# Performance work log

Measured on AMD Instinct MI355X. Metric: run time of the kernel, lower is better.

The kernel has to match this reference:

```python
import jax, jax.numpy as jnp
import numpy as np

M_TIME = 64      # signal model output length (time points)
N_DICT = 20000   # dictionary entries
B_VOX = 8192     # voxels / batch


def setup_inputs() -> dict:
    key = jax.random.key(0)
    k = jax.random.split(key, 6)
    input_real = jax.random.normal(k[0], (M_TIME, B_VOX), jnp.float32)
    input_imag = jax.random.normal(k[1], (M_TIME, B_VOX), jnp.float32)
    # raw dictionary signals, then normalize columns as append() does
    yr = jax.random.normal(k[2], (M_TIME, N_DICT), jnp.float32)
    yi = jax.random.normal(k[3], (M_TIME, N_DICT), jnp.float32)
    norm = jnp.sqrt(jnp.sum(yr * yr + yi * yi, axis=0))  # (N,)
    inverse_norm_y = 1.0 / norm
    y_real = yr * inverse_norm_y
    y_imag = yi * inverse_norm_y
    x_t1 = jax.random.uniform(k[4], (N_DICT,), jnp.float32, 0.1, 3.0)
    x_t2 = jax.random.uniform(k[5], (N_DICT,), jnp.float32, 0.01, 0.5)
    return {
        'input_real': input_real, 'input_imag': input_imag,
        'y_real': y_real, 'y_imag': y_imag,
        'inverse_norm_y': inverse_norm_y, 'x_t1': x_t1, 'x_t2': x_t2,
    }


def reference(input_real, input_imag, y_real, y_imag, inverse_norm_y, x_t1, x_t2):
    # |<y_n, s_b>|^2 for complex y and complex input, via 4 real GEMMs (as in the
    # original module): sim[n, b]
    sim = (jnp.einsum('mb,mn->nb', input_real, y_real) ** 2
           + jnp.einsum('mb,mn->nb', input_real, y_imag) ** 2
           + jnp.einsum('mb,mn->nb', input_imag, y_real) ** 2
           + jnp.einsum('mb,mn->nb', input_imag, y_imag) ** 2)
    idx = jnp.argmax(sim, axis=0)  # (B,)
    # scale = sum_m conj(y[:, idx]) * input * inverse_norm_y[idx]
    yr = y_real[:, idx]   # (M, B)
    yi = y_imag[:, idx]   # (M, B)
    inv = inverse_norm_y[idx]  # (B,)
    scale_r = jnp.sum(yr * input_real + yi * input_imag, axis=0) * inv
    scale_i = jnp.sum(yr * input_imag - yi * input_real, axis=0) * inv
    # returns (scale, t1, t2) with complex scale split into real/imag, stacked (4, B)
    return jnp.stack([scale_r, scale_i, x_t1[idx], x_t2[idx]])
```

## Files before the change

kernel.cpp:

```cpp
#include <hip/hip_runtime.h>
#include <hip/hip_bf16.h>
#include <stdint.h>

#define M_TIME 64
#define N_DICT 20000
#define B_VOX  8192

#define NTILES 313

typedef _Float16 v8h __attribute__((ext_vector_type(8)));
typedef float    v4f __attribute__((ext_vector_type(4)));
typedef float    v2f __attribute__((ext_vector_type(2)));

__device__ __forceinline__ unsigned long long u64max(unsigned long long a, unsigned long long b) { return a > b ? a : b; }
__device__ __forceinline__ unsigned umin32(unsigned a, unsigned b) { return a < b ? a : b; }
__device__ __forceinline__ unsigned umax32(unsigned a, unsigned b) { return a > b ? a : b; }
__device__ __forceinline__ unsigned umed3(unsigned a, unsigned b, unsigned c) {
    unsigned d;
    asm("v_med3_u32 %0, %1, %2, %3" : "=v"(d) : "v"(a), "v"(b), "v"(c));
    return d;
}

__global__ __launch_bounds__(256) void split_y(
    const float* __restrict__ yr, const float* __restrict__ yi,
    v8h* __restrict__ yp)
{
    const int u = blockIdx.x * 256 + threadIdx.x;
    const int n_l = u & 63;
    const int j   = (u >> 6) & 7;
    const int T   = (u >> 9) % NTILES;
    const int arr = u / (NTILES * 512);
    if (arr > 1) return;
    const float* P = arr ? yi : yr;
    const int n_g = T * 64 + n_l;
    v8h V;
#pragma unroll
    for (int c = 0; c < 8; ++c) {
        float v = 0.f;
        if (n_g < N_DICT) v = P[(j * 8 + c) * N_DICT + n_g];
        V[c] = (_Float16)v;
    }
    const int fr = (arr * 2 + (j >> 2)) * 4 + (j & 3);
    yp[((size_t)T * 16 + fr) * 64 + n_l] = V;
}

__global__ __launch_bounds__(256, 2) void gemm_pre(
    const float* __restrict__ ir, const float* __restrict__ ii,
    const v8h* __restrict__ yp,
    unsigned* __restrict__ cand, int tpc, int slots)
{
    __shared__ unsigned xm[4][4][16][2];

    const int tid  = threadIdx.x;
    const int wave = tid >> 6, lane = tid & 63;
    const int quad = lane >> 4, col = lane & 15;
    const int vox_w = blockIdx.x * 64;
    const int chunk = blockIdx.y;
    const int T0 = chunk * tpc;
    const int T1 = (T0 + tpc < NTILES) ? T0 + tpc : NTILES;

    v8h fh[2][4][2];
#pragma unroll
    for (int arr = 0; arr < 2; ++arr) {
        const float* P = arr ? ii : ir;
#pragma unroll
        for (int bt = 0; bt < 4; ++bt) {
            const int b = vox_w + bt * 16 + col;
#pragma unroll
            for (int h = 0; h < 2; ++h) {
                v8h H;
#pragma unroll
                for (int j = 0; j < 8; ++j) {
                    const int k = h * 32 + quad * 8 + j;
                    H[j] = (_Float16)P[k * B_VOX + b];
                }
                fh[arr][bt][h] = H;
            }
        }
    }

    v8h yf[2][2];
    auto loadf = [&](int T) {
        const v8h* yv = (const v8h*)((const char*)yp + (size_t)T * 16384);
        const int nrow = wave * 16 + col;
#pragma unroll
        for (int ri = 0; ri < 2; ++ri)
#pragma unroll
            for (int h = 0; h < 2; ++h)
                yf[ri][h] = yv[((ri * 2 + h) * 4 + quad) * 64 + nrow];
    };

    const v4f zc = {0.f, 0.f, 0.f, 0.f};
    unsigned t2a[4] = {0u, 0u, 0u, 0u}, t2b[4] = {0u, 0u, 0u, 0u};

    loadf(T0);
    for (int T = T0; T < T1; ++T) {
        const int tl = T - T0;
        v4f acc[4][4];
#define MF(A, B, C) __builtin_amdgcn_mfma_f32_16x16x32_f16(A, B, C, 0, 0, 0)
#pragma unroll
        for (int bt = 0; bt < 4; ++bt) {
            acc[bt][0] = MF(yf[0][0], fh[0][bt][0], zc);
            acc[bt][1] = MF(yf[1][0], fh[0][bt][0], zc);
            acc[bt][2] = MF(yf[0][0], fh[1][bt][0], zc);
            acc[bt][3] = MF(yf[1][0], fh[1][bt][0], zc);
        }
#pragma unroll
        for (int bt = 0; bt < 4; ++bt) {
            acc[bt][0] = MF(yf[0][1], fh[0][bt][1], acc[bt][0]);
            acc[bt][1] = MF(yf[1][1], fh[0][bt][1], acc[bt][1]);
            acc[bt][2] = MF(yf[0][1], fh[1][bt][1], acc[bt][2]);
            acc[bt][3] = MF(yf[1][1], fh[1][bt][1], acc[bt][3]);
        }
#undef MF
        if (T + 1 < T1) loadf(T + 1);

        const unsigned base = 0x1FFFu
            - (unsigned)(tl * 64 + wave * 16 + quad * 4);
#pragma unroll
        for (int bt = 0; bt < 4; ++bt) {
            v2f s01, s23;
            {
                const v2f p0 = __builtin_shufflevector(acc[bt][0], acc[bt][0], 0, 1);
                const v2f p1 = __builtin_shufflevector(acc[bt][1], acc[bt][1], 0, 1);
                const v2f p2 = __builtin_shufflevector(acc[bt][2], acc[bt][2], 0, 1);
                const v2f p3 = __builtin_shufflevector(acc[bt][3], acc[bt][3], 0, 1);
                v2f s = p0 * p0;
                s = __builtin_elementwise_fma(p1, p1, s);
                s = __builtin_elementwise_fma(p2, p2, s);
                s = __builtin_elementwise_fma(p3, p3, s);
                s01 = s;
            }
            {
                const v2f p0 = __builtin_shufflevector(acc[bt][0], acc[bt][0], 2, 3);
                const v2f p1 = __builtin_shufflevector(acc[bt][1], acc[bt][1], 2, 3);
                const v2f p2 = __builtin_shufflevector(acc[bt][2], acc[bt][2], 2, 3);
                const v2f p3 = __builtin_shufflevector(acc[bt][3], acc[bt][3], 2, 3);
                v2f s = p0 * p0;
                s = __builtin_elementwise_fma(p1, p1, s);
                s = __builtin_elementwise_fma(p2, p2, s);
                s = __builtin_elementwise_fma(p3, p3, s);
                s23 = s;
            }
#pragma unroll
            for (int r = 0; r < 4; ++r) {
                const float s = (r < 2) ? s01[r] : s23[r - 2];
                const unsigned pb = (__float_as_uint(s) & 0xFFFFE000u)
                                  | (base - (unsigned)r);
                const unsigned nb = umed3(pb, t2a[bt], t2b[bt]);
                t2a[bt] = umax32(pb, t2a[bt]);
                t2b[bt] = nb;
            }
        }
    }

    unsigned fa1[4], fa2[4];
#pragma unroll
    for (int bt = 0; bt < 4; ++bt) {
        unsigned a1 = t2a[bt], a2 = t2b[bt];
#pragma unroll
        for (int d = 16; d <= 32; d <<= 1) {
            unsigned b1 = (unsigned)__shfl_xor((int)a1, d, 64);
            unsigned b2 = (unsigned)__shfl_xor((int)a2, d, 64);
            unsigned mn = umin32(a1, b1);
            a1 = umax32(a1, b1);
            a2 = umax32(mn, umax32(a2, b2));
        }
        fa1[bt] = a1; fa2[bt] = a2;
    }
    if (lane < 16) {
#pragma unroll
        for (int bt = 0; bt < 4; ++bt) {
            xm[wave][bt][lane][0] = fa1[bt];
            xm[wave][bt][lane][1] = fa2[bt];
        }
    }
    __syncthreads();
    if (wave == 0 && lane < 16) {
#pragma unroll
        for (int bt = 0; bt < 4; ++bt) {
            unsigned m1 = 0u, m2 = 0u;
#pragma unroll
            for (int w = 0; w < 4; ++w) {
                const unsigned b1 = xm[w][bt][lane][0];
                const unsigned b2 = xm[w][bt][lane][1];
                m2 = umax32(m2, umax32(b2, umin32(m1, b1)));
                m1 = umax32(m1, b1);
            }
            const size_t vox = vox_w + bt * 16 + lane;
            cand[vox * slots + chunk * 2 + 0] = m1;
            cand[vox * slots + chunk * 2 + 1] = m2;
        }
    }
}

__global__ __launch_bounds__(256) void rescore_finish(
    const float* __restrict__ ir, const float* __restrict__ ii,
    const float* __restrict__ yr, const float* __restrict__ yi,
    const float* __restrict__ inv, const float* __restrict__ x1,
    const float* __restrict__ x2,
    const unsigned* __restrict__ cand, int slots, int tpc,
    float* __restrict__ out)
{
    const int tid  = threadIdx.x;
    const int vox  = blockIdx.x * 4 + (tid >> 6);
    const int slot = tid & 63;

    unsigned p = (slot < slots) ? cand[(size_t)vox * slots + slot] : 0u;
    float sa = __uint_as_float(p & 0xFFFFE000u);
    const int chunkc = slot >> 1;
    const int nn = chunkc * tpc * 64 + (0x1FFF - (int)(p & 0x1FFFu));

    float amax = sa;
#pragma unroll
    for (int d = 1; d <= 32; d <<= 1) amax = fmaxf(amax, __shfl_xor(amax, d, 64));

    unsigned long long q = 0ull;
    float rr = 0.f, ri = 0.f, s1 = 0.f, s2 = 0.f;
    const bool active = (slot < slots) && (nn >= 0) && (nn < N_DICT)
                     && (sa >= 0.97f * amax);
    if (active) {
        for (int m = 0; m < M_TIME; ++m) {
            float a  = yr[(size_t)m * N_DICT + nn];
            float c  = yi[(size_t)m * N_DICT + nn];
            float vr = ir[m * B_VOX + vox];
            float vi = ii[m * B_VOX + vox];
            rr = fmaf(vr, a, rr); ri = fmaf(vr, c, ri);
            s1 = fmaf(vi, a, s1); s2 = fmaf(vi, c, s2);
        }
        float s = fmaf(rr, rr, fmaf(ri, ri, fmaf(s1, s1, s2 * s2)));
        q = (((unsigned long long)__float_as_uint(s)) << 32)
          | (unsigned long long)(0xFFFFFFFFu - (unsigned)nn);
    }
    unsigned long long qm = q;
#pragma unroll
    for (int d = 1; d <= 32; d <<= 1) qm = u64max(qm, __shfl_xor(qm, d, 64));

    if (active && q == qm && qm != 0ull) {
        float ss = inv[nn];
        out[0 * B_VOX + vox] = (rr + s2) * ss;
        out[1 * B_VOX + vox] = (s1 - ri) * ss;
        out[2 * B_VOX + vox] = x1[nn];
        out[3 * B_VOX + vox] = x2[nn];
    }
}

__global__ __launch_bounds__(256, 3) void argmax_naive(
    const float* __restrict__ ir, const float* __restrict__ ii,
    const float* __restrict__ yr, const float* __restrict__ yi,
    int* __restrict__ idxout)
{
    int b = blockIdx.x * 256 + threadIdx.x;
    float bs = -1.0f; int bn = 0;
    for (int n = 0; n < N_DICT; ++n) {
        float a_rr = 0.f, a_ri = 0.f, a_s1 = 0.f, a_s2 = 0.f;
        for (int m = 0; m < M_TIME; ++m) {
            float a = yr[m * N_DICT + n], c = yi[m * N_DICT + n];
            float vr = ir[m * B_VOX + b], vi = ii[m * B_VOX + b];
            a_rr = fmaf(vr, a, a_rr); a_ri = fmaf(vr, c, a_ri);
            a_s1 = fmaf(vi, a, a_s1); a_s2 = fmaf(vi, c, a_s2);
        }
        float sim = fmaf(a_rr, a_rr, fmaf(a_ri, a_ri, fmaf(a_s1, a_s1, a_s2 * a_s2)));
        if (sim > bs) { bs = sim; bn = n; }
    }
    idxout[b] = bn;
}

__global__ void finish_k(const float* __restrict__ ir, const float* __restrict__ ii,
                         const float* __restrict__ yr, const float* __restrict__ yi,
                         const float* __restrict__ inv, const float* __restrict__ x1,
                         const float* __restrict__ x2,
                         const int* __restrict__ idxin, float* __restrict__ out)
{
    int b = blockIdx.x * blockDim.x + threadIdx.x;
    int idx = idxin[b];
    float ar = 0.f, ai = 0.f;
    for (int m = 0; m < M_TIME; ++m) {
        float a  = yr[(size_t)m * N_DICT + idx];
        float c  = yi[(size_t)m * N_DICT + idx];
        float vr = ir[m * B_VOX + b];
        float vi = ii[m * B_VOX + b];
        ar = fmaf(a, vr, ar); ar = fmaf(c, vi, ar);
        ai = fmaf(a, vi, ai); ai = fmaf(-c, vr, ai);
    }
    float s = inv[idx];
    out[0 * B_VOX + b] = ar * s;
    out[1 * B_VOX + b] = ai * s;
    out[2 * B_VOX + b] = x1[idx];
    out[3 * B_VOX + b] = x2[idx];
}

extern "C" void kernel_launch(void* const* d_in, const int* in_sizes, int n_in,
                              void* d_out, int out_size, void* d_ws, size_t ws_size,
                              hipStream_t stream) {
    const float* ir  = (const float*)d_in[0];
    const float* ii  = (const float*)d_in[1];
    const float* yr  = (const float*)d_in[2];
    const float* yi  = (const float*)d_in[3];
    const float* inv = (const float*)d_in[4];
    const float* x1  = (const float*)d_in[5];
    const float* x2  = (const float*)d_in[6];
    float* out = (float*)d_out;

    const size_t yp_bytes = (size_t)NTILES * 16384;

    int CH = 0;
    for (int c = 32; c >= 4; c >>= 1) {
        size_t cand_bytes = (size_t)B_VOX * (2 * c) * sizeof(unsigned);
        if (ws_size >= cand_bytes + yp_bytes) { CH = c; break; }
    }

    if (CH > 0) {
        const int slots = 2 * CH;
        const int tpc   = (NTILES + CH - 1) / CH;
        unsigned* cand = (unsigned*)d_ws;
        v8h* yp = (v8h*)((char*)d_ws + (size_t)B_VOX * slots * sizeof(unsigned));

        const int units = 2 * NTILES * 512;
        split_y<<<(units + 255) / 256, 256, 0, stream>>>(yr, yi, yp);
        gemm_pre<<<dim3(B_VOX / 64, CH), 256, 0, stream>>>(ir, ii, yp, cand, tpc, slots);
        rescore_finish<<<B_VOX / 4, 256, 0, stream>>>(ir, ii, yr, yi, inv, x1, x2,
                                                      cand, slots, tpc, out);
    } else {
        int* idxo = (int*)(out + 3 * B_VOX);
        argmax_naive<<<B_VOX / 256, 256, 0, stream>>>(ir, ii, yr, yi, idxo);
        finish_k<<<B_VOX / 256, 256, 0, stream>>>(ir, ii, yr, yi,
                                                  inv, x1, x2, idxo, out);
    }
}
```

Measured before the change: 186.2 us.

## Switch similarity GEMM to 32x32x16 MFMA with 2x2 wave tiling

```diff
diff --git a/kernel.cpp b/kernel.cpp
--- a/kernel.cpp
+++ b/kernel.cpp
@@ -11,6 +11,7 @@
 typedef _Float16 v8h __attribute__((ext_vector_type(8)));
 typedef float    v4f __attribute__((ext_vector_type(4)));
 typedef float    v2f __attribute__((ext_vector_type(2)));
+typedef float    v16f __attribute__((ext_vector_type(16)));
 
 __device__ __forceinline__ unsigned long long u64max(unsigned long long a, unsigned long long b) { return a > b ? a : b; }
 __device__ __forceinline__ unsigned umin32(unsigned a, unsigned b) { return a < b ? a : b; }
@@ -49,148 +50,126 @@
     const v8h* __restrict__ yp,
     unsigned* __restrict__ cand, int tpc, int slots)
 {
-    __shared__ unsigned xm[4][4][16][2];
+    __shared__ unsigned xm[2][32][2];
 
     const int tid  = threadIdx.x;
     const int wave = tid >> 6, lane = tid & 63;
-    const int quad = lane >> 4, col = lane & 15;
+    const int col  = lane & 31, hk = lane >> 5;
+    const int vh   = wave >> 1, nh = wave & 1;
     const int vox_w = blockIdx.x * 64;
     const int chunk = blockIdx.y;
     const int T0 = chunk * tpc;
     const int T1 = (T0 + tpc < NTILES) ? T0 + tpc : NTILES;
 
-    v8h fh[2][4][2];
+    v8h fh[2][4];
 #pragma unroll
     for (int arr = 0; arr < 2; ++arr) {
         const float* P = arr ? ii : ir;
-#pragma unroll
-        for (int bt = 0; bt < 4; ++bt) {
-            const int b = vox_w + bt * 16 + col;
-#pragma unroll
-            for (int h = 0; h < 2; ++h) {
-                v8h H;
-#pragma unroll
-                for (int j = 0; j < 8; ++j) {
-                    const int k = h * 32 + quad * 8 + j;
-                    H[j] = (_Float16)P[k * B_VOX + b];
-                }
-                fh[arr][bt][h] = H;
+        const int b = vox_w + vh * 32 + col;
+#pragma unroll
+        for (int ks = 0; ks < 4; ++ks) {
+            v8h H;
+#pragma unroll
+            for (int j = 0; j < 8; ++j) {
+                const int k = ks * 16 + hk * 8 + j;
+                H[j] = (_Float16)P[k * B_VOX + b];
             }
+            fh[arr][ks] = H;
         }
     }
 
-    v8h yf[2][2];
+    v8h yf[2][4];
     auto loadf = [&](int T) {
         const v8h* yv = (const v8h*)((const char*)yp + (size_t)T * 16384);
-        const int nrow = wave * 16 + col;
+        const int nr = nh * 32 + col;
 #pragma unroll
         for (int ri = 0; ri < 2; ++ri)
 #pragma unroll
-            for (int h = 0; h < 2; ++h)
-                yf[ri][h] = yv[((ri * 2 + h) * 4 + quad) * 64 + nrow];
+            for (int ks = 0; ks < 4; ++ks)
+                yf[ri][ks] = yv[(ri * 8 + ks * 2 + hk) * 64 + nr];
     };
 
-    const v4f zc = {0.f, 0.f, 0.f, 0.f};
-    unsigned t2a[4] = {0u, 0u, 0u, 0u}, t2b[4] = {0u, 0u, 0u, 0u};
+    const v16f zc16 = {0.f,0.f,0.f,0.f,0.f,0.f,0.f,0.f,
+                       0.f,0.f,0.f,0.f,0.f,0.f,0.f,0.f};
+    unsigned t2a[4] = {0u,0u,0u,0u}, t2b[4] = {0u,0u,0u,0u};
 
     loadf(T0);
     for (int T = T0; T < T1; ++T) {
         const int tl = T - T0;
-        v4f acc[4][4];
-#define MF(A, B, C) __builtin_amdgcn_mfma_f32_16x16x32_f16(A, B, C, 0, 0, 0)
-#pragma unroll
-        for (int bt = 0; bt < 4; ++bt) {
-            acc[bt][0] = MF(yf[0][0], fh[0][bt][0], zc);
-            acc[bt][1] = MF(yf[1][0], fh[0][bt][0], zc);
-            acc[bt][2] = MF(yf[0][0], fh[1][bt][0], zc);
-            acc[bt][3] = MF(yf[1][0], fh[1][bt][0], zc);
-        }
-#pragma unroll
-        for (int bt = 0; bt < 4; ++bt) {
-            acc[bt][0] = MF(yf[0][1], fh[0][bt][1], acc[bt][0]);
-            acc[bt][1] = MF(yf[1][1], fh[0][bt][1], acc[bt][1]);
-            acc[bt][2] = MF(yf[0][1], fh[1][bt][1], acc[bt][2]);
-            acc[bt][3] = MF(yf[1][1], fh[1][bt][1], acc[bt][3]);
+        v16f acc0, acc1, acc2, acc3;
+#define MF(A, B, C) __builtin_amdgcn_mfma_f32_32x32x16_f16(A, B, C, 0, 0, 0)
+        acc0 = MF(yf[0][0], fh[0][0], zc16);
+        acc1 = MF(yf[1][0], fh[0][0], zc16);
+        acc2 = MF(yf[0][0], fh[1][0], zc16);
+        acc3 = MF(yf[1][0], fh[1][0], zc16);
+#pragma unroll
+        for (int ks = 1; ks < 4; ++ks) {
+            acc0 = MF(yf[0][ks], fh[0][ks], acc0);
+            acc1 = MF(yf[1][ks], fh[0][ks], acc1);
+            acc2 = MF(yf[0][ks], fh[1][ks], acc2);
+            acc3 = MF(yf[1][ks], fh[1][ks], acc3);
         }
 #undef MF
         if (T + 1 < T1) loadf(T + 1);
 
-        const unsigned base = 0x1FFFu
-            - (unsigned)(tl * 64 + wave * 16 + quad * 4);
-#pragma unroll
-        for (int bt = 0; bt < 4; ++bt) {
-            v2f s01, s23;
-            {
-                const v2f p0 = __builtin_shufflevector(acc[bt][0], acc[bt][0], 0, 1);
-                const v2f p1 = __builtin_shufflevector(acc[bt][1], acc[bt][1], 0, 1);
-                const v2f p2 = __builtin_shufflevector(acc[bt][2], acc[bt][2], 0, 1);
-                const v2f p3 = __builtin_shufflevector(acc[bt][3], acc[bt][3], 0, 1);
-                v2f s = p0 * p0;
-                s = __builtin_elementwise_fma(p1, p1, s);
-                s = __builtin_elementwise_fma(p2, p2, s);
-                s = __builtin_elementwise_fma(p3, p3, s);
-                s01 = s;
-            }
-            {
-                const v2f p0 = __builtin_shufflevector(acc[bt][0], acc[bt][0], 2, 3);
-                const v2f p1 = __builtin_shufflevector(acc[bt][1], acc[bt][1], 2, 3);
-                const v2f p2 = __builtin_shufflevector(acc[bt][2], acc[bt][2], 2, 3);
-                const v2f p3 = __builtin_shufflevector(acc[bt][3], acc[bt][3], 2, 3);
-                v2f s = p0 * p0;
-                s = __builtin_elementwise_fma(p1, p1, s);
-                s = __builtin_elementwise_fma(p2, p2, s);
-                s = __builtin_elementwise_fma(p3, p3, s);
-                s23 = s;
-            }
-#pragma unroll
-            for (int r = 0; r < 4; ++r) {
-                const float s = (r < 2) ? s01[r] : s23[r - 2];
-                const unsigned pb = (__float_as_uint(s) & 0xFFFFE000u)
-                                  | (base - (unsigned)r);
-                const unsigned nb = umed3(pb, t2a[bt], t2b[bt]);
-                t2a[bt] = umax32(pb, t2a[bt]);
-                t2b[bt] = nb;
-            }
-        }
-    }
-
-    unsigned fa1[4], fa2[4];
-#pragma unroll
-    for (int bt = 0; bt < 4; ++bt) {
-        unsigned a1 = t2a[bt], a2 = t2b[bt];
-#pragma unroll
-        for (int d = 16; d <= 32; d <<= 1) {
-            unsigned b1 = (unsigned)__shfl_xor((int)a1, d, 64);
-            unsigned b2 = (unsigned)__shfl_xor((int)a2, d, 64);
-            unsigned mn = umin32(a1, b1);
-            a1 = umax32(a1, b1);
-            a2 = umax32(mn, umax32(a2, b2));
-        }
-        fa1[bt] = a1; fa2[bt] = a2;
-    }
-    if (lane < 16) {
-#pragma unroll
-        for (int bt = 0; bt < 4; ++bt) {
-            xm[wave][bt][lane][0] = fa1[bt];
-            xm[wave][bt][lane][1] = fa2[bt];
-        }
-    }
+        const unsigned invb = 0x1FFFu
+            - (unsigned)(tl * 64 + nh * 32 + hk * 4);
+#define EPI(G) { \
+        const unsigned baseg = invb - (unsigned)(8 * G); \
+        v2f s01, s23; \
+        { v2f p0 = __builtin_shufflevector(acc0, acc0, 4*G+0, 4*G+1); \
+          v2f p1 = __builtin_shufflevector(acc1, acc1, 4*G+0, 4*G+1); \
+          v2f p2 = __builtin_shufflevector(acc2, acc2, 4*G+0, 4*G+1); \
+          v2f p3 = __builtin_shufflevector(acc3, acc3, 4*G+0, 4*G+1); \
+          v2f s = p0 * p0; \
+          s = __builtin_elementwise_fma(p1, p1, s); \
+          s = __builtin_elementwise_fma(p2, p2, s); \
+          s = __builtin_elementwise_fma(p3, p3, s); \
+          s01 = s; } \
+        { v2f p0 = __builtin_shufflevector(acc0, acc0, 4*G+2, 4*G+3); \
+          v2f p1 = __builtin_shufflevector(acc1, acc1, 4*G+2, 4*G+3); \
+          v2f p2 = __builtin_shufflevector(acc2, acc2, 4*G+2, 4*G+3); \
+          v2f p3 = __builtin_shufflevector(acc3, acc3, 4*G+2, 4*G+3); \
+          v2f s = p0 * p0; \
+          s = __builtin_elementwise_fma(p1, p1, s); \
+          s = __builtin_elementwise_fma(p2, p2, s); \
+          s = __builtin_elementwise_fma(p3, p3, s); \
+          s23 = s; } \
+        _Pragma("unroll") \
+        for (int r = 0; r < 4; ++r) { \
+            const float sv = (r < 2) ? s01[r] : s23[r - 2]; \
+            const unsigned pb = (__float_as_uint(sv) & 0xFFFFE000u) \
+                              | (baseg - (unsigned)r); \
+            t2b[G] = umed3(pb, t2a[G], t2b[G]); \
+            t2a[G] = umax32(pb, t2a[G]); } }
+        EPI(0) EPI(1) EPI(2) EPI(3)
+#undef EPI
+    }
+
+    unsigned a1 = t2a[0], a2 = t2b[0];
+#pragma unroll
+    for (int g = 1; g < 4; ++g) {
+        unsigned lo = umin32(a1, t2a[g]);
+        a1 = umax32(a1, t2a[g]);
+        a2 = umax32(umax32(a2, t2b[g]), lo);
+    }
+    {
+        unsigned b1 = (unsigned)__shfl_xor((int)a1, 32, 64);
+        unsigned b2 = (unsigned)__shfl_xor((int)a2, 32, 64);
+        unsigned mn = umin32(a1, b1);
+        a1 = umax32(a1, b1);
+        a2 = umax32(mn, umax32(a2, b2));
+    }
+    if (nh == 1 && lane < 32) { xm[vh][lane][0] = a1; xm[vh][lane][1] = a2; }
     __syncthreads();
-    if (wave == 0 && lane < 16) {
-#pragma unroll
-        for (int bt = 0; bt < 4; ++bt) {
-            unsigned m1 = 0u, m2 = 0u;
-#pragma unroll
-            for (int w = 0; w < 4; ++w) {
-                const unsigned b1 = xm[w][bt][lane][0];
-                const unsigned b2 = xm[w][bt][lane][1];
-                m2 = umax32(m2, umax32(b2, umin32(m1, b1)));
-                m1 = umax32(m1, b1);
-            }
-            const size_t vox = vox_w + bt * 16 + lane;
-            cand[vox * slots + chunk * 2 + 0] = m1;
-            cand[vox * slots + chunk * 2 + 1] = m2;
-        }
+    if (nh == 0 && lane < 32) {
+        const unsigned b1 = xm[vh][lane][0];
+        const unsigned b2 = xm[vh][lane][1];
+        const unsigned m1 = umax32(a1, b1);
+        const unsigned m2 = umax32(umin32(a1, b1), umax32(a2, b2));
+        const size_t vox = vox_w + vh * 32 + lane;
+        cand[vox * slots + chunk * 2 + 0] = m1;
+        cand[vox * slots + chunk * 2 + 1] = m2;
     }
 }
 
```

Result: slower. 209.3 us (+12.4%).
